# Kernel optimization log

Measured on AMD Instinct MI355X. Metric: run time of the kernel, lower is better.

The kernel has to match this reference:

```python
import jax, jax.numpy as jnp
import numpy as np

D_MODEL = 512
D_AUX = 64
B, E = 8, 2048


def setup_inputs() -> dict:
    key = jax.random.key(0)
    ks = jax.random.split(key, 12)
    x = jax.random.normal(ks[0], (B, E, D_MODEL), dtype=jnp.float32)
    query_aux = jax.random.normal(ks[1], (B, E, D_AUX), dtype=jnp.float32)
    key_aux = jax.random.normal(ks[2], (B, E, D_AUX), dtype=jnp.float32)
    adjacency_mask = jax.random.randint(ks[3], (B, E, E), 0, 2, dtype=jnp.int32)
    merge_coefficients = jax.random.uniform(ks[4], (B, E, E), dtype=jnp.float32)
    # learned parameters of IrregularityAwareAttention (nn.Linear weights stored
    # as (out, in) in torch; we keep (in, out) for x @ W)
    s = 1.0 / np.sqrt(D_MODEL)
    Wq = jax.random.uniform(ks[5], (D_MODEL, D_MODEL), minval=-s, maxval=s, dtype=jnp.float32)
    bq = jax.random.uniform(ks[6], (D_MODEL,), minval=-s, maxval=s, dtype=jnp.float32)
    Wk = jax.random.uniform(ks[7], (D_MODEL, D_MODEL), minval=-s, maxval=s, dtype=jnp.float32)
    bk = jax.random.uniform(ks[8], (D_MODEL,), minval=-s, maxval=s, dtype=jnp.float32)
    Wv = jax.random.uniform(ks[9], (D_MODEL, D_MODEL), minval=-s, maxval=s, dtype=jnp.float32)
    bv = jax.random.uniform(ks[10], (D_MODEL,), minval=-s, maxval=s, dtype=jnp.float32)
    threshold = jnp.float32(0.5)
    return {
        "x": x, "query_aux": query_aux, "key_aux": key_aux,
        "adjacency_mask": adjacency_mask, "merge_coefficients": merge_coefficients,
        "Wq": Wq, "bq": bq, "Wk": Wk, "bk": bk, "Wv": Wv, "bv": bv,
        "threshold": threshold,
    }


def reference(x, query_aux, key_aux, adjacency_mask, merge_coefficients,
              Wq, bq, Wk, bk, Wv, bv, threshold):
    d_model = x.shape[-1]
    scale = jnp.asarray(d_model, x.dtype) ** 0.5
    q = x @ Wq + bq                      # (B, E, D)
    k = x @ Wk + bk
    v = x @ Wv + bv
    scores = jnp.einsum("bed,bfd->bef", q, k) / scale   # (B, E, E)

    aux_scale = jnp.asarray(key_aux.shape[-1], x.dtype) ** 0.5
    scores_aux = jnp.einsum("bed,bfd->bef", query_aux, key_aux) / aux_scale

    non_zero_mask = scores_aux != 0
    positive_mask = scores > threshold
    merge_mask = positive_mask & non_zero_mask
    blended = (1.0 - merge_coefficients) * scores + merge_coefficients * scores_aux
    scores = jnp.where(merge_mask, blended, scores)

    mask_value = jnp.finfo(scores.dtype).min
    scores = jnp.where(adjacency_mask == 0, mask_value, scores)

    attn = jax.nn.softmax(scores, axis=-1)
    return jnp.einsum("bef,bfd->bed", attn, v)
```

## Files before the change

kernel.cpp:

```cpp
#include <hip/hip_runtime.h>

#define E2 2048
#define DM 512

typedef __attribute__((ext_vector_type(8))) _Float16 half8;
typedef __attribute__((ext_vector_type(4))) _Float16 half4;
typedef __attribute__((ext_vector_type(8))) short short8;
typedef __attribute__((ext_vector_type(4))) short shortx4;
typedef __attribute__((ext_vector_type(4))) float floatx4;

#define WAITV4 asm volatile("s_waitcnt vmcnt(4)" ::: "memory")
#define WAITV2 asm volatile("s_waitcnt vmcnt(2)" ::: "memory")
#define WAITV0 asm volatile("s_waitcnt vmcnt(0)" ::: "memory")
#define WAITL0 asm volatile("s_waitcnt lgkmcnt(0)" ::: "memory")
#define BARRIER __builtin_amdgcn_s_barrier()
#define SCHEDB __builtin_amdgcn_sched_barrier(0)

__device__ __forceinline__ void stage_tile8(const _Float16* __restrict__ g, int stride,
                                            _Float16* lds, int tid) {
  const int r0 = tid >> 2;
  const int cs = ((tid & 3) ^ (r0 & 3)) * 8;
  const int wbase = (tid >> 6) * 512;
  const _Float16* gp = g + (size_t)r0 * stride + cs;
  __builtin_amdgcn_global_load_lds(
      (const __attribute__((address_space(1))) unsigned int*)gp,
      (__attribute__((address_space(3))) unsigned int*)(lds + wbase), 16, 0, 0);
}

__device__ __forceinline__ void mfma8(const _Float16* As, const _Float16* Bs,
                                      floatx4 acc[4][2], int wm, int wn, int lane) {
  const int m16 = lane & 15, quad = lane >> 4;
  const int sq = (quad ^ (m16 & 3)) * 8;
  half8 a[4];
#pragma unroll
  for (int i = 0; i < 4; ++i)
    a[i] = *(const half8*)(As + (wm * 64 + i * 16 + m16) * 32 + sq);
#pragma unroll
  for (int j = 0; j < 2; ++j) {
    const half8 b = *(const half8*)(Bs + (wn * 32 + j * 16 + m16) * 32 + sq);
#pragma unroll
    for (int i = 0; i < 4; ++i)
      acc[i][j] = __builtin_amdgcn_mfma_f32_16x16x32_f16(a[i], b, acc[i][j], 0, 0, 0);
  }
}

__device__ __forceinline__ void mfma24(const _Float16* Ah, const _Float16* Al,
                                       const _Float16* Bh, const _Float16* Bl,
                                       floatx4 acc[4][2], int wm, int wn, int lane) {
  const int m16 = lane & 15, quad = lane >> 4;
  const int sq = (quad ^ (m16 & 3)) * 8;
  half8 ah[4], al[4];
#pragma unroll
  for (int i = 0; i < 4; ++i) {
    const int off = (wm * 64 + i * 16 + m16) * 32 + sq;
    ah[i] = *(const half8*)(Ah + off);
    al[i] = *(const half8*)(Al + off);
  }
#pragma unroll
  for (int j = 0; j < 2; ++j) {
    const int off = (wn * 32 + j * 16 + m16) * 32 + sq;
    const half8 bh = *(const half8*)(Bh + off);
    const half8 bl = *(const half8*)(Bl + off);
#pragma unroll
    for (int i = 0; i < 4; ++i) {
      acc[i][j] = __builtin_amdgcn_mfma_f32_16x16x32_f16(ah[i], bh, acc[i][j], 0, 0, 0);
      acc[i][j] = __builtin_amdgcn_mfma_f32_16x16x32_f16(al[i], bh, acc[i][j], 0, 0, 0);
      acc[i][j] = __builtin_amdgcn_mfma_f32_16x16x32_f16(ah[i], bl, acc[i][j], 0, 0, 0);
    }
  }
}

__global__ void split_conv_k(const float* __restrict__ src, _Float16* __restrict__ hi,
                             _Float16* __restrict__ lo, float scale, int n8) {
  int i = blockIdx.x * blockDim.x + threadIdx.x;
  const int stride = gridDim.x * blockDim.x;
  const float4* s4 = (const float4*)src;
  for (; i < n8; i += stride) {
    const float4 u = s4[2 * i], v = s4[2 * i + 1];
    const float g[8] = {u.x, u.y, u.z, u.w, v.x, v.y, v.z, v.w};
    half8 h, l;
#pragma unroll
    for (int t = 0; t < 8; ++t) {
      const float gv = g[t] * scale;
      const _Float16 hv = (_Float16)gv;
      h[t] = hv;
      l[t] = (_Float16)(gv - (float)hv);
    }
    ((half8*)hi)[i] = h;
    ((half8*)lo)[i] = l;
  }
}

__global__ void conv_k(const float* __restrict__ src, _Float16* __restrict__ dst, int n8) {
  int i = blockIdx.x * blockDim.x + threadIdx.x;
  const int stride = gridDim.x * blockDim.x;
  const float4* s4 = (const float4*)src;
  for (; i < n8; i += stride) {
    const float4 u = s4[2 * i], v = s4[2 * i + 1];
    const float g[8] = {u.x, u.y, u.z, u.w, v.x, v.y, v.z, v.w};
    half8 h;
#pragma unroll
    for (int t = 0; t < 8; ++t) h[t] = (_Float16)g[t];
    ((half8*)dst)[i] = h;
  }
}

__global__ void transw_k(const float* __restrict__ Wq, const float* __restrict__ Wk,
                         const float* __restrict__ Wv, _Float16* __restrict__ Wth,
                         _Float16* __restrict__ Wtl) {
  const int z = blockIdx.z;
  const float* W = (z == 0) ? Wq : (z == 1) ? Wk : Wv;
  __shared__ float t[32][33];
  const int n0 = blockIdx.x * 32, k0 = blockIdx.y * 32;
  const int tx = threadIdx.x, ty = threadIdx.y;
#pragma unroll
  for (int i = 0; i < 32; i += 8) t[ty + i][tx] = W[(size_t)(k0 + ty + i) * DM + n0 + tx];
  __syncthreads();
  const size_t zb = (size_t)z * DM * DM;
#pragma unroll
  for (int i = 0; i < 32; i += 8) {
    const float g = t[tx][ty + i] * 64.0f;
    const _Float16 h = (_Float16)g;
    const size_t o = zb + (size_t)(n0 + ty + i) * DM + (k0 + tx);
    Wth[o] = h;
    Wtl[o] = (_Float16)(g - (float)h);
  }
}

__global__ __launch_bounds__(512, 4) void qkv_k(
    const _Float16* __restrict__ xh, const _Float16* __restrict__ xl,
    const _Float16* __restrict__ Wth, const _Float16* __restrict__ Wtl,
    const float* __restrict__ bqp, const float* __restrict__ bkp,
    const float* __restrict__ bvp,
    _Float16* __restrict__ qh, _Float16* __restrict__ ql,
    _Float16* __restrict__ kh, _Float16* __restrict__ kl,
    _Float16* __restrict__ vT) {
  __shared__ _Float16 Ah[2][4096], Al[2][4096], Bh[2][4096], Bl[2][4096];
  const int tid = threadIdx.x, lane = tid & 63, wv = tid >> 6;
  const int wm = wv >> 2, wn = wv & 3;
  const int flat = blockIdx.x + 128 * (blockIdx.y + 4 * blockIdx.z);
  const int s = flat & 7, k = flat >> 3;
  const int bm = s * 16 + (k & 15);
  const int bnz = k >> 4;
  const int bn = bnz & 3, z = bnz >> 2;
  const bool split = (z < 2);
  const _Float16* Ash = xh + (size_t)bm * 128 * DM;
  const _Float16* Asl = xl + (size_t)bm * 128 * DM;
  const _Float16* Bsh = Wth + ((size_t)z * DM + bn * 128) * DM;
  const _Float16* Bsl = Wtl + ((size_t)z * DM + bn * 128) * DM;
  floatx4 acc[4][2];
  const floatx4 z4 = {0.f, 0.f, 0.f, 0.f};
#pragma unroll
  for (int i = 0; i < 4; ++i)
#pragma unroll
    for (int j = 0; j < 2; ++j) acc[i][j] = z4;

  stage_tile8(Ash, DM, Ah[0], tid);
  stage_tile8(Bsh, DM, Bh[0], tid);
  if (split) { stage_tile8(Asl, DM, Al[0], tid); stage_tile8(Bsl, DM, Bl[0], tid); }
  for (int kt = 0; kt < 16; ++kt) {
    const int cur = kt & 1, nxt = cur ^ 1;
    if (kt < 15) {
      const int ko = (kt + 1) * 32;
      stage_tile8(Ash + ko, DM, Ah[nxt], tid);
      stage_tile8(Bsh + ko, DM, Bh[nxt], tid);
      if (split) {
        stage_tile8(Asl + ko, DM, Al[nxt], tid);
        stage_tile8(Bsl + ko, DM, Bl[nxt], tid);
        WAITV4;
      } else {
        WAITV2;
      }
    } else {
      WAITV0;
    }
    BARRIER;
    SCHEDB;
    if (split) mfma24(Ah[cur], Al[cur], Bh[cur], Bl[cur], acc, wm, wn, lane);
    else       mfma8(Ah[cur], Bh[cur], acc, wm, wn, lane);
    WAITL0;
    BARRIER;
    SCHEDB;
  }
  const int m16 = lane & 15, quad = lane >> 4;
  const float* bias = (z == 0) ? bqp : (z == 1) ? bkp : bvp;
  if (split) {
    _Float16* oh = (z == 0) ? qh : kh;
    _Float16* ol = (z == 0) ? ql : kl;
#pragma unroll
    for (int j = 0; j < 2; ++j) {
      const int n = bn * 128 + wn * 32 + j * 16 + m16;
      const float bb = bias[n];
#pragma unroll
      for (int i = 0; i < 4; ++i) {
        const int m = bm * 128 + wm * 64 + i * 16 + quad * 4;
#pragma unroll
        for (int r = 0; r < 4; ++r) {
          const float val = acc[i][j][r] * (1.0f / 256.0f) + bb;
          const float v8 = val * 8.0f;
          const _Float16 h = (_Float16)v8;
          const _Float16 l = (_Float16)(v8 - (float)h);
          const size_t o = (size_t)(m + r) * DM + n;
          oh[o] = h; ol[o] = l;
        }
      }
    }
  } else {
#pragma unroll
    for (int j = 0; j < 2; ++j) {
      const int n = bn * 128 + wn * 32 + j * 16 + m16;
      const float bb = bias[n];
#pragma unroll
      for (int i = 0; i < 4; ++i) {
        const int m = bm * 128 + wm * 64 + i * 16 + quad * 4;
        const int bidx = m >> 11, e0 = m & 2047;
        half4 pk;
#pragma unroll
        for (int r = 0; r < 4; ++r)
          pk[r] = (_Float16)(acc[i][j][r] * (1.0f / 256.0f) + bb);
        *(half4*)(vT + ((size_t)bidx * DM + n) * E2 + e0) = pk;
      }
    }
  }
}

__global__ __launch_bounds__(512, 4) void scores_k(
    const _Float16* __restrict__ qh, const _Float16* __restrict__ ql,
    const _Float16* __restrict__ kh, const _Float16* __restrict__ kl,
    const _Float16* __restrict__ qah, const _Float16* __restrict__ kah,
    const float* __restrict__ mc,
    const float* __restrict__ thrp, unsigned short* __restrict__ sc) {
  __shared__ _Float16 S[32768];
  _Float16* const AhB = S;
  _Float16* const AlB = S + 8192;
  _Float16* const BhB = S + 16384;
  _Float16* const BlB = S + 24576;
  const int tid = threadIdx.x, lane = tid & 63, wv = tid >> 6;
  const int wm = wv >> 2, wn = wv & 3;
  const int bf = blockIdx.x, be = blockIdx.y, b = blockIdx.z;
  const _Float16* Ash = qh + ((size_t)b * E2 + be * 128) * DM;
  const _Float16* Asl = ql + ((size_t)b * E2 + be * 128) * DM;
  const _Float16* Bsh = kh + ((size_t)b * E2 + bf * 128) * DM;
  const _Float16* Bsl = kl + ((size_t)b * E2 + bf * 128) * DM;
  floatx4 accm[4][2];
  const floatx4 z4 = {0.f, 0.f, 0.f, 0.f};
#pragma unroll
  for (int i = 0; i < 4; ++i)
#pragma unroll
    for (int j = 0; j < 2; ++j) accm[i][j] = z4;

  stage_tile8(Ash, DM, AhB, tid);
  stage_tile8(Bsh, DM, BhB, tid);
  stage_tile8(Asl, DM, AlB, tid);
  stage_tile8(Bsl, DM, BlB, tid);
  for (int kt = 0; kt < 16; ++kt) {
    const int cur = kt & 1, nxt = cur ^ 1;
    if (kt < 15) {
      const int ko = (kt + 1) * 32;
      stage_tile8(Ash + ko, DM, AhB + nxt * 4096, tid);
      stage_tile8(Bsh + ko, DM, BhB + nxt * 4096, tid);
      stage_tile8(Asl + ko, DM, AlB + nxt * 4096, tid);
      stage_tile8(Bsl + ko, DM, BlB + nxt * 4096, tid);
      WAITV4;
    } else {
      WAITV0;
    }
    BARRIER;
    SCHEDB;
    mfma24(AhB + cur * 4096, AlB + cur * 4096, BhB + cur * 4096, BlB + cur * 4096,
           accm, wm, wn, lane);
    WAITL0;
    BARRIER;
    SCHEDB;
  }
  floatx4 acca[4][2];
#pragma unroll
  for (int i = 0; i < 4; ++i)
#pragma unroll
    for (int j = 0; j < 2; ++j) acca[i][j] = z4;
  const _Float16* A2 = qah + ((size_t)b * E2 + be * 128) * 64;
  const _Float16* B2 = kah + ((size_t)b * E2 + bf * 128) * 64;
  stage_tile8(A2, 64, AhB, tid);
  stage_tile8(B2, 64, BhB, tid);
  stage_tile8(A2 + 32, 64, AhB + 4096, tid);
  stage_tile8(B2 + 32, 64, BhB + 4096, tid);
  __syncthreads();
  mfma8(AhB, BhB, acca, wm, wn, lane);
  mfma8(AhB + 4096, BhB + 4096, acca, wm, wn, lane);

  float* const sL = (float*)S;
  _Float16* const saL = S + 16896;
  const float thr = *thrp;
  const int m16 = lane & 15, quad = lane >> 4;
  const size_t rowbase0 = (size_t)b * E2 + be * 128;
#pragma unroll
  for (int h = 0; h < 2; ++h) {
    __syncthreads();
    if (wm == h) {
#pragma unroll
      for (int j = 0; j < 2; ++j) {
        const int cl = wn * 32 + j * 16 + m16;
#pragma unroll
        for (int i = 0; i < 4; ++i) {
#pragma unroll
          for (int r = 0; r < 4; ++r) {
            const int rl = i * 16 + quad * 4 + r;
            sL[rl * 132 + cl] = accm[i][j][r] * (0.015625f * 0.044194173824159216f);
            saL[rl * 132 + cl] = (_Float16)(acca[i][j][r] * 0.125f);
          }
        }
      }
    }
    __syncthreads();
#pragma unroll
    for (int g = 0; g < 4; ++g) {
      const int tf = g * 2048 + tid * 4;
      const int rl = tf >> 7, cl = tf & 127;
      const size_t idx = (rowbase0 + h * 64 + rl) * E2 + bf * 128 + cl;
      const float4 c4 = *(const float4*)(mc + idx);
      const float4 s4v = *(const float4*)(sL + rl * 132 + cl);
      const half4 sa4 = *(const half4*)(saL + rl * 132 + cl);
      const float ss[4] = {s4v.x, s4v.y, s4v.z, s4v.w};
      const float cc[4] = {c4.x, c4.y, c4.z, c4.w};
      shortx4 o;
#pragma unroll
      for (int t = 0; t < 4; ++t) {
        float s = ss[t];
        const float sa = (float)sa4[t];
        if (sa != 0.0f && s > thr) s = (1.0f - cc[t]) * s + cc[t] * sa;
        union { _Float16 hh; unsigned short u; } u;
        u.hh = (_Float16)s;
        o[t] = (short)u.u;
      }
      *(shortx4*)(sc + idx) = o;
    }
  }
}

__global__ __launch_bounds__(256) void smax_k(unsigned short* __restrict__ sc,
                                              const int* __restrict__ adj) {
  const size_t row = blockIdx.x;
  unsigned short* p = sc + row * E2;
  const int* arow = adj + row * E2;
  const int tid = threadIdx.x, lane = tid & 63, wv = tid >> 6;
  const short8 raw = *(const short8*)(p + tid * 8);
  const int4 a0 = *(const int4*)(arow + tid * 8);
  const int4 a1 = *(const int4*)(arow + tid * 8 + 4);
  const int aa[8] = {a0.x, a0.y, a0.z, a0.w, a1.x, a1.y, a1.z, a1.w};
  float f[8];
#pragma unroll
  for (int t = 0; t < 8; ++t) {
    union { _Float16 h; short s; } u; u.s = raw[t];
    f[t] = aa[t] ? (float)u.h : -65504.0f;
  }
  float mx = f[0];
#pragma unroll
  for (int t = 1; t < 8; ++t) mx = fmaxf(mx, f[t]);
#pragma unroll
  for (int o = 32; o > 0; o >>= 1) mx = fmaxf(mx, __shfl_xor(mx, o, 64));
  __shared__ float red[8];
  if (lane == 0) red[wv] = mx;
  __syncthreads();
  mx = fmaxf(fmaxf(red[0], red[1]), fmaxf(red[2], red[3]));
  float ef[8], sum = 0.f;
#pragma unroll
  for (int t = 0; t < 8; ++t) { ef[t] = __expf(f[t] - mx); sum += ef[t]; }
#pragma unroll
  for (int o = 32; o > 0; o >>= 1) sum += __shfl_xor(sum, o, 64);
  if (lane == 0) red[4 + wv] = sum;
  __syncthreads();
  sum = (red[4] + red[5]) + (red[6] + red[7]);
  const float inv = 1.0f / sum;
  short8 ov;
#pragma unroll
  for (int t = 0; t < 8; ++t) {
    union { _Float16 h; short s; } u;
    u.h = (_Float16)(ef[t] * inv);
    ov[t] = u.s;
  }
  *(short8*)(p + tid * 8) = ov;
}

__global__ __launch_bounds__(512, 6) void pv_k(
    const _Float16* __restrict__ at, const _Float16* __restrict__ vT,
    float* __restrict__ out) {
  __shared__ _Float16 As[3][4096], Bs[3][4096];
  const int tid = threadIdx.x, lane = tid & 63, wv = tid >> 6;
  const int wm = wv >> 2, wn = wv & 3;
  const int flat = blockIdx.x + 4 * blockIdx.y + 64 * blockIdx.z;
  const int virt = (flat & 7) * 64 + (flat >> 3);
  const int bd = virt & 3, be = (virt >> 2) & 15, b = virt >> 6;
  const _Float16* Asrc = at + ((size_t)b * E2 + be * 128) * E2;
  const _Float16* Bsrc = vT + ((size_t)b * DM + bd * 128) * E2;
  floatx4 acc[4][2];
  const floatx4 z4 = {0.f, 0.f, 0.f, 0.f};
#pragma unroll
  for (int i = 0; i < 4; ++i)
#pragma unroll
    for (int j = 0; j < 2; ++j) acc[i][j] = z4;
  stage_tile8(Asrc, E2, As[0], tid);
  stage_tile8(Bsrc, E2, Bs[0], tid);
  int cur = 0;
  for (int kt = 0; kt < 64; ++kt) {
    const int nxt = (cur == 2) ? 0 : cur + 1;
    if (kt < 63) {
      const int ko = (kt + 1) * 32;
      stage_tile8(Asrc + ko, E2, As[nxt], tid);
      stage_tile8(Bsrc + ko, E2, Bs[nxt], tid);
      WAITV2;
    } else {
      WAITV0;
    }
    BARRIER;
    SCHEDB;
    mfma8(As[cur], Bs[cur], acc, wm, wn, lane);
    WAITL0;
    cur = nxt;
  }
  const int m16 = lane & 15, quad = lane >> 4;
#pragma unroll
  for (int j = 0; j < 2; ++j) {
    const int d = bd * 128 + wn * 32 + j * 16 + m16;
#pragma unroll
    for (int i = 0; i < 4; ++i) {
      const int e0 = be * 128 + wm * 64 + i * 16 + quad * 4;
#pragma unroll
      for (int r = 0; r < 4; ++r)
        out[((size_t)b * E2 + e0 + r) * DM + d] = acc[i][j][r];
    }
  }
}

extern "C" void kernel_launch(void* const* d_in, const int* in_sizes, int n_in,
                              void* d_out, int out_size, void* d_ws, size_t ws_size,
                              hipStream_t stream) {
  const float* x   = (const float*)d_in[0];
  const float* qa  = (const float*)d_in[1];
  const float* ka  = (const float*)d_in[2];
  const int*   adj = (const int*)d_in[3];
  const float* mc  = (const float*)d_in[4];
  const float* Wq  = (const float*)d_in[5];
  const float* bq  = (const float*)d_in[6];
  const float* Wk  = (const float*)d_in[7];
  const float* bk  = (const float*)d_in[8];
  const float* Wv  = (const float*)d_in[9];
  const float* bv  = (const float*)d_in[10];
  const float* thr = (const float*)d_in[11];
  float* out = (float*)d_out;
  char* w = (char*)d_ws;
  const size_t MiB = 1ull << 20;
  _Float16* xh  = (_Float16*)(w + 0 * MiB);
  _Float16* xl  = (_Float16*)(w + 16 * MiB);
  _Float16* qhp = (_Float16*)(w + 32 * MiB);
  _Float16* qlp = (_Float16*)(w + 48 * MiB);
  _Float16* khp = (_Float16*)(w + 64 * MiB);
  _Float16* klp = (_Float16*)(w + 80 * MiB);
  _Float16* vT  = (_Float16*)(w + 96 * MiB);
  _Float16* Wth = (_Float16*)(w + 112 * MiB);
  _Float16* Wtl = (_Float16*)(w + 114 * MiB);
  _Float16* qah = (_Float16*)(w + 116 * MiB);
  _Float16* kah = (_Float16*)(w + 118 * MiB);
  unsigned short* sc = (unsigned short*)(w + 120 * MiB);

  split_conv_k<<<2048, 256, 0, stream>>>(x, xh, xl, 4.0f, (8 * E2 * DM) / 8);
  conv_k<<<256, 256, 0, stream>>>(qa, qah, (8 * E2 * 64) / 8);
  conv_k<<<256, 256, 0, stream>>>(ka, kah, (8 * E2 * 64) / 8);
  transw_k<<<dim3(16, 16, 3), dim3(32, 8), 0, stream>>>(Wq, Wk, Wv, Wth, Wtl);
  qkv_k<<<dim3(128, 4, 3), 512, 0, stream>>>(xh, xl, Wth, Wtl, bq, bk, bv,
                                             qhp, qlp, khp, klp, vT);
  scores_k<<<dim3(16, 16, 8), 512, 0, stream>>>(qhp, qlp, khp, klp, qah, kah,
                                                mc, thr, sc);
  smax_k<<<16384, 256, 0, stream>>>(sc, adj);
  pv_k<<<dim3(4, 16, 8), 512, 0, stream>>>((const _Float16*)sc, vT, out);
}
```

Measured before the change: 564.1 us.

## Merge prep kernels, simplify GEMM syncs to __syncthreads, two rows per softmax block

Three small conversion/transposition kernels are folded into one prep_k launch to cut launch overhead. The hand-tuned vmcnt waits and barriers in the qkv and scores GEMM loops are replaced with a plain __syncthreads at the end of each iteration. The softmax kernel now handles two rows per 512-thread block. Dropping the explicit vmcnt waits lets the compiler insert full waits, which may remove the overlap between prefetch and MFMA work.

```diff
diff --git a/kernel.cpp b/kernel.cpp
--- a/kernel.cpp
+++ b/kernel.cpp
@@ -9,7 +9,6 @@
 typedef __attribute__((ext_vector_type(4))) short shortx4;
 typedef __attribute__((ext_vector_type(4))) float floatx4;
 
-#define WAITV4 asm volatile("s_waitcnt vmcnt(4)" ::: "memory")
 #define WAITV2 asm volatile("s_waitcnt vmcnt(2)" ::: "memory")
 #define WAITV0 asm volatile("s_waitcnt vmcnt(0)" ::: "memory")
 #define WAITL0 asm volatile("s_waitcnt lgkmcnt(0)" ::: "memory")
@@ -91,39 +90,45 @@
   }
 }
 
-__global__ void conv_k(const float* __restrict__ src, _Float16* __restrict__ dst, int n8) {
-  int i = blockIdx.x * blockDim.x + threadIdx.x;
-  const int stride = gridDim.x * blockDim.x;
-  const float4* s4 = (const float4*)src;
-  for (; i < n8; i += stride) {
-    const float4 u = s4[2 * i], v = s4[2 * i + 1];
-    const float g[8] = {u.x, u.y, u.z, u.w, v.x, v.y, v.z, v.w};
-    half8 h;
-#pragma unroll
-    for (int t = 0; t < 8; ++t) h[t] = (_Float16)g[t];
-    ((half8*)dst)[i] = h;
-  }
-}
-
-__global__ void transw_k(const float* __restrict__ Wq, const float* __restrict__ Wk,
-                         const float* __restrict__ Wv, _Float16* __restrict__ Wth,
-                         _Float16* __restrict__ Wtl) {
-  const int z = blockIdx.z;
-  const float* W = (z == 0) ? Wq : (z == 1) ? Wk : Wv;
-  __shared__ float t[32][33];
-  const int n0 = blockIdx.x * 32, k0 = blockIdx.y * 32;
-  const int tx = threadIdx.x, ty = threadIdx.y;
-#pragma unroll
-  for (int i = 0; i < 32; i += 8) t[ty + i][tx] = W[(size_t)(k0 + ty + i) * DM + n0 + tx];
-  __syncthreads();
-  const size_t zb = (size_t)z * DM * DM;
-#pragma unroll
-  for (int i = 0; i < 32; i += 8) {
-    const float g = t[tx][ty + i] * 64.0f;
-    const _Float16 h = (_Float16)g;
-    const size_t o = zb + (size_t)(n0 + ty + i) * DM + (k0 + tx);
-    Wth[o] = h;
-    Wtl[o] = (_Float16)(g - (float)h);
+__global__ void prep_k(const float* __restrict__ Wq, const float* __restrict__ Wk,
+                       const float* __restrict__ Wv, _Float16* __restrict__ Wth,
+                       _Float16* __restrict__ Wtl,
+                       const float* __restrict__ qa, _Float16* __restrict__ qah,
+                       const float* __restrict__ ka, _Float16* __restrict__ kah) {
+  const int bid = blockIdx.x, tid = threadIdx.x;
+  if (bid < 768) {
+    const int z = bid >> 8;
+    const float* W = (z == 0) ? Wq : (z == 1) ? Wk : Wv;
+    __shared__ float t[32][33];
+    const int n0 = (bid & 15) * 32, k0 = ((bid >> 4) & 15) * 32;
+    const int tx = tid & 31, ty = tid >> 5;
+#pragma unroll
+    for (int i = 0; i < 32; i += 8) t[ty + i][tx] = W[(size_t)(k0 + ty + i) * DM + n0 + tx];
+    __syncthreads();
+    const size_t zb = (size_t)z * DM * DM;
+#pragma unroll
+    for (int i = 0; i < 32; i += 8) {
+      const float g = t[tx][ty + i] * 64.0f;
+      const _Float16 h = (_Float16)g;
+      const size_t o = zb + (size_t)(n0 + ty + i) * DM + (k0 + tx);
+      Wth[o] = h;
+      Wtl[o] = (_Float16)(g - (float)h);
+    }
+  } else {
+    const bool isQ = bid < 1024;
+    const float* src = isQ ? qa : ka;
+    _Float16* dst = isQ ? qah : kah;
+    const int n8 = (8 * E2 * 64) / 8;
+    int i = (bid & 255) * 256 + tid;
+    const float4* s4 = (const float4*)src;
+    for (; i < n8; i += 256 * 256) {
+      const float4 u = s4[2 * i], v = s4[2 * i + 1];
+      const float g[8] = {u.x, u.y, u.z, u.w, v.x, v.y, v.z, v.w};
+      half8 h;
+#pragma unroll
+      for (int t = 0; t < 8; ++t) h[t] = (_Float16)g[t];
+      ((half8*)dst)[i] = h;
+    }
   }
 }
 
@@ -158,29 +163,18 @@
   stage_tile8(Ash, DM, Ah[0], tid);
   stage_tile8(Bsh, DM, Bh[0], tid);
   if (split) { stage_tile8(Asl, DM, Al[0], tid); stage_tile8(Bsl, DM, Bl[0], tid); }
+  __syncthreads();
   for (int kt = 0; kt < 16; ++kt) {
     const int cur = kt & 1, nxt = cur ^ 1;
     if (kt < 15) {
       const int ko = (kt + 1) * 32;
       stage_tile8(Ash + ko, DM, Ah[nxt], tid);
       stage_tile8(Bsh + ko, DM, Bh[nxt], tid);
-      if (split) {
-        stage_tile8(Asl + ko, DM, Al[nxt], tid);
-        stage_tile8(Bsl + ko, DM, Bl[nxt], tid);
-        WAITV4;
-      } else {
-        WAITV2;
-      }
-    } else {
-      WAITV0;
-    }
-    BARRIER;
-    SCHEDB;
+      if (split) { stage_tile8(Asl + ko, DM, Al[nxt], tid); stage_tile8(Bsl + ko, DM, Bl[nxt], tid); }
+    }
     if (split) mfma24(Ah[cur], Al[cur], Bh[cur], Bl[cur], acc, wm, wn, lane);
     else       mfma8(Ah[cur], Bh[cur], acc, wm, wn, lane);
-    WAITL0;
-    BARRIER;
-    SCHEDB;
+    __syncthreads();
   }
   const int m16 = lane & 15, quad = lane >> 4;
   const float* bias = (z == 0) ? bqp : (z == 1) ? bkp : bvp;
@@ -253,6 +247,7 @@
   stage_tile8(Bsh, DM, BhB, tid);
   stage_tile8(Asl, DM, AlB, tid);
   stage_tile8(Bsl, DM, BlB, tid);
+  __syncthreads();
   for (int kt = 0; kt < 16; ++kt) {
     const int cur = kt & 1, nxt = cur ^ 1;
     if (kt < 15) {
@@ -261,17 +256,10 @@
       stage_tile8(Bsh + ko, DM, BhB + nxt * 4096, tid);
       stage_tile8(Asl + ko, DM, AlB + nxt * 4096, tid);
       stage_tile8(Bsl + ko, DM, BlB + nxt * 4096, tid);
-      WAITV4;
-    } else {
-      WAITV0;
-    }
-    BARRIER;
-    SCHEDB;
+    }
     mfma24(AhB + cur * 4096, AlB + cur * 4096, BhB + cur * 4096, BlB + cur * 4096,
            accm, wm, wn, lane);
-    WAITL0;
-    BARRIER;
-    SCHEDB;
+    __syncthreads();
   }
   floatx4 acca[4][2];
 #pragma unroll
@@ -337,48 +325,56 @@
   }
 }
 
-__global__ __launch_bounds__(256) void smax_k(unsigned short* __restrict__ sc,
+__global__ __launch_bounds__(512) void smax_k(unsigned short* __restrict__ sc,
                                               const int* __restrict__ adj) {
-  const size_t row = blockIdx.x;
+  const int tid = threadIdx.x, lane = tid & 63, wv = tid >> 6;
+  const int rh = tid >> 8;
+  const int t = tid & 255;
+  const size_t row = (size_t)blockIdx.x * 2 + rh;
   unsigned short* p = sc + row * E2;
   const int* arow = adj + row * E2;
-  const int tid = threadIdx.x, lane = tid & 63, wv = tid >> 6;
-  const short8 raw = *(const short8*)(p + tid * 8);
-  const int4 a0 = *(const int4*)(arow + tid * 8);
-  const int4 a1 = *(const int4*)(arow + tid * 8 + 4);
+  const short8 raw = *(const short8*)(p + t * 8);
+  const int4 a0 = *(const int4*)(arow + t * 8);
+  const int4 a1 = *(const int4*)(arow + t * 8 + 4);
   const int aa[8] = {a0.x, a0.y, a0.z, a0.w, a1.x, a1.y, a1.z, a1.w};
   float f[8];
 #pragma unroll
-  for (int t = 0; t < 8; ++t) {
-    union { _Float16 h; short s; } u; u.s = raw[t];
-    f[t] = aa[t] ? (float)u.h : -65504.0f;
+  for (int u = 0; u < 8; ++u) {
+    union { _Float16 h; short s; } c; c.s = raw[u];
+    f[u] = aa[u] ? (float)c.h : -65504.0f;
   }
   float mx = f[0];
 #pragma unroll
-  for (int t = 1; t < 8; ++t) mx = fmaxf(mx, f[t]);
+  for (int u = 1; u < 8; ++u) mx = fmaxf(mx, f[u]);
 #pragma unroll
   for (int o = 32; o > 0; o >>= 1) mx = fmaxf(mx, __shfl_xor(mx, o, 64));
-  __shared__ float red[8];
+  __shared__ float red[16];
   if (lane == 0) red[wv] = mx;
   __syncthreads();
-  mx = fmaxf(fmaxf(red[0], red[1]), fmaxf(red[2], red[3]));
+  {
+    const int base = rh * 4;
+    mx = fmaxf(fmaxf(red[base + 0], red[base + 1]), fmaxf(red[base + 2], red[base + 3]));
+  }
   float ef[8], sum = 0.f;
 #pragma unroll
-  for (int t = 0; t < 8; ++t) { ef[t] = __expf(f[t] - mx); sum += ef[t]; }
+  for (int u = 0; u < 8; ++u) { ef[u] = __expf(f[u] - mx); sum += ef[u]; }
 #pragma unroll
   for (int o = 32; o > 0; o >>= 1) sum += __shfl_xor(sum, o, 64);
-  if (lane == 0) red[4 + wv] = sum;
+  if (lane == 0) red[8 + wv] = sum;
   __syncthreads();
-  sum = (red[4] + red[5]) + (red[6] + red[7]);
+  {
+    const int base = 8 + rh * 4;
+    sum = (red[base + 0] + red[base + 1]) + (red[base + 2] + red[base + 3]);
+  }
   const float inv = 1.0f / sum;
   short8 ov;
 #pragma unroll
-  for (int t = 0; t < 8; ++t) {
-    union { _Float16 h; short s; } u;
-    u.h = (_Float16)(ef[t] * inv);
-    ov[t] = u.s;
-  }
-  *(short8*)(p + tid * 8) = ov;
+  for (int u = 0; u < 8; ++u) {
+    union { _Float16 h; short s; } c;
+    c.h = (_Float16)(ef[u] * inv);
+    ov[u] = c.s;
+  }
+  *(short8*)(p + t * 8) = ov;
 }
 
 __global__ __launch_bounds__(512, 6) void pv_k(
@@ -463,13 +459,11 @@
   unsigned short* sc = (unsigned short*)(w + 120 * MiB);
 
   split_conv_k<<<2048, 256, 0, stream>>>(x, xh, xl, 4.0f, (8 * E2 * DM) / 8);
-  conv_k<<<256, 256, 0, stream>>>(qa, qah, (8 * E2 * 64) / 8);
-  conv_k<<<256, 256, 0, stream>>>(ka, kah, (8 * E2 * 64) / 8);
-  transw_k<<<dim3(16, 16, 3), dim3(32, 8), 0, stream>>>(Wq, Wk, Wv, Wth, Wtl);
+  prep_k<<<1280, 256, 0, stream>>>(Wq, Wk, Wv, Wth, Wtl, qa, qah, ka, kah);
   qkv_k<<<dim3(128, 4, 3), 512, 0, stream>>>(xh, xl, Wth, Wtl, bq, bk, bv,
                                              qhp, qlp, khp, klp, vT);
   scores_k<<<dim3(16, 16, 8), 512, 0, stream>>>(qhp, qlp, khp, klp, qah, kah,
                                                 mc, thr, sc);
-  smax_k<<<16384, 256, 0, stream>>>(sc, adj);
+  smax_k<<<8192, 512, 0, stream>>>(sc, adj);
   pv_k<<<dim3(4, 16, 8), 512, 0, stream>>>((const _Float16*)sc, vT, out);
 }
```

Result: no change. 558.8 us (-0.9%).
